# Optimization experiments

Measured on AMD Instinct MI355X. Metric: run time of the kernel, lower is better.

Reference implementation:

```python
import jax, jax.numpy as jnp
import numpy as np

N = 50000
E = 800000
F_IN = 1433
H = 256
C = 7


def setup_inputs() -> dict:
    key = jax.random.key(0)
    ks = jax.random.split(key, 8)
    x = jax.random.normal(ks[0], (N, F_IN), dtype=jnp.float32)
    edge_index = jax.random.randint(ks[1], (2, E), 0, N, dtype=jnp.int32)
    # glorot init for linear weights
    def glorot(k, fan_in, fan_out):
        s = jnp.sqrt(6.0 / (fan_in + fan_out)).astype(jnp.float32)
        return jax.random.uniform(k, (fan_in, fan_out), jnp.float32, -s, s)
    W1 = glorot(ks[2], F_IN, H)
    W2 = glorot(ks[3], H, H)
    W3 = glorot(ks[4], H, C)
    b1 = jnp.zeros((H,), jnp.float32)
    b2 = jnp.zeros((H,), jnp.float32)
    b3 = jnp.zeros((C,), jnp.float32)
    return {"x": x, "edge_index": edge_index, "W1": W1, "b1": b1,
            "W2": W2, "b2": b2, "W3": W3, "b3": b3}


def _gcn_norm(edge_index, num_nodes):
    # add self-loops, edge_weight = 1, symmetric normalization
    row = jnp.concatenate([edge_index[0], jnp.arange(num_nodes, dtype=edge_index.dtype)])
    col = jnp.concatenate([edge_index[1], jnp.arange(num_nodes, dtype=edge_index.dtype)])
    w = jnp.ones(row.shape[0], dtype=jnp.float32)
    deg = jax.ops.segment_sum(w, col, num_segments=num_nodes)  # degree on target (col)
    dinv = jnp.where(deg > 0, jax.lax.rsqrt(deg), 0.0)
    norm = dinv[row] * dinv[col]  # [E+N]
    return row, col, norm


def _gcn_layer(x, W, b, row, col, norm, num_nodes):
    h = x @ W                                   # [N, F_out]
    msg = h[row] * norm[:, None]                # gather + scale, [E+N, F_out]
    out = jax.ops.segment_sum(msg, col, num_segments=num_nodes)  # scatter-add
    return out + b


def reference(x, edge_index, W1, b1, W2, b2, W3, b3):
    row, col, norm = _gcn_norm(edge_index, N)
    h = jax.nn.relu(_gcn_layer(x, W1, b1, row, col, norm, N))
    h = jax.nn.relu(_gcn_layer(h, W2, b2, row, col, norm, N))
    h = _gcn_layer(h, W3, b3, row, col, norm, N)
    return jax.nn.log_softmax(h, axis=1)
```

## Files before the change

kernel.cpp:

```cpp
#include <hip/hip_runtime.h>
#include <math.h>

#define NNODES 50000
#define NEDGES 800000
#define FIN    1433
#define KP1    1472
#define HDIM   256
#define NCLS   7
#define MPAD   50048

typedef __attribute__((ext_vector_type(8))) short short8;
typedef __attribute__((ext_vector_type(4))) float f32x4;

__device__ __forceinline__ unsigned short f2bf(float f) {
    unsigned u = __builtin_bit_cast(unsigned, f);
    u += 0x7fffu + ((u >> 16) & 1u);
    return (unsigned short)(u >> 16);
}

__device__ __forceinline__ float bf2f(unsigned short u) {
    unsigned v = ((unsigned)u) << 16;
    return __builtin_bit_cast(float, v);
}

__device__ __forceinline__ void gl2lds16(const void* g, void* l) {
    __builtin_amdgcn_global_load_lds(
        (const __attribute__((address_space(1))) unsigned int*)g,
        (__attribute__((address_space(3))) unsigned int*)l, 16, 0, 0);
}

__device__ __forceinline__ f32x4 ld4u(const float* p) {
    f32x4 v; __builtin_memcpy(&v, p, 16); return v;
}


__global__ void count_kernel(const int* __restrict__ col, int* __restrict__ cnt, int E) {
    int e = blockIdx.x * blockDim.x + threadIdx.x;
    if (e < E) atomicAdd(&cnt[col[e]], 1);
}

#define SCAN_BS 512

__global__ __launch_bounds__(SCAN_BS) void scan_part(const int* __restrict__ cnt,
                                                     int* __restrict__ bsum, int n) {
    __shared__ int red[SCAN_BS];
    int t = threadIdx.x;
    int i = blockIdx.x * SCAN_BS + t;
    red[t] = (i < n) ? cnt[i] : 0;
    __syncthreads();
    for (int off = SCAN_BS / 2; off > 0; off >>= 1) {
        if (t < off) red[t] += red[t + off];
        __syncthreads();
    }
    if (t == 0) bsum[blockIdx.x] = red[0];
}

__global__ __launch_bounds__(128) void scan_top(int* __restrict__ bsum, int nb) {
    __shared__ int s[128];
    int t = threadIdx.x;
    int v = (t < nb) ? bsum[t] : 0;
    s[t] = v;
    __syncthreads();
    for (int off = 1; off < 128; off <<= 1) {
        int u = (t >= off) ? s[t - off] : 0;
        __syncthreads();
        s[t] += u;
        __syncthreads();
    }
    if (t < nb) bsum[t] = s[t] - v;
}

__global__ __launch_bounds__(SCAN_BS) void scan_apply(const int* __restrict__ cnt,
                                                      const int* __restrict__ bsum,
                                                      int* __restrict__ rp,
                                                      float* __restrict__ dinv,
                                                      int n, int total) {
    __shared__ int s[SCAN_BS];
    int t = threadIdx.x;
    int i = blockIdx.x * SCAN_BS + t;
    int v = (i < n) ? cnt[i] : 0;
    s[t] = v;
    __syncthreads();
    for (int off = 1; off < SCAN_BS; off <<= 1) {
        int u = (t >= off) ? s[t - off] : 0;
        __syncthreads();
        s[t] += u;
        __syncthreads();
    }
    if (i < n) {
        rp[i] = bsum[blockIdx.x] + s[t] - v;
        dinv[i] = rsqrtf((float)(v + 1));
    }
    if (i == n) rp[n] = total;
}

__global__ void fill_kernel(const int* __restrict__ row, const int* __restrict__ col,
                            const int* __restrict__ rp, int* __restrict__ cur,
                            int2* __restrict__ csrw,
                            const float* __restrict__ dinv, int E) {
    int e = blockIdx.x * blockDim.x + threadIdx.x;
    if (e < E) {
        int c = col[e], r = row[e];
        int pos = rp[c] + atomicAdd(&cur[c], 1);
        csrw[pos] = make_int2(r, __float_as_int(dinv[r] * dinv[c]));
    }
}


__global__ void cast_wt2(const float* __restrict__ W1, const float* __restrict__ W2,
                         unsigned short* __restrict__ w1t, unsigned short* __restrict__ w2t) {
    int idx = blockIdx.x * blockDim.x + threadIdx.x;
    if (idx < HDIM * KP1) {
        int n = idx / KP1, k = idx % KP1;
        w1t[idx] = f2bf((k < FIN) ? W1[(size_t)k * HDIM + n] : 0.f);
    } else {
        int j = idx - HDIM * KP1;
        if (j < HDIM * HDIM) {
            int n = j / HDIM, k = j % HDIM;
            w2t[j] = f2bf(W2[(size_t)k * HDIM + n]);
        }
    }
}


__global__ __launch_bounds__(256) void gemm1_fused(const float* __restrict__ X,
                                                   const unsigned short* __restrict__ Bt,
                                                   unsigned short* __restrict__ C) {
    __shared__ __align__(16) unsigned short As[64 * 64];
    __shared__ __align__(16) unsigned short Bs[256 * 64];
    const int tid = threadIdx.x;
    const int wave = tid >> 6, lane = tid & 63;
    const int m0 = blockIdx.x * 64;
    const int wn = wave * 64;
    const int kq = lane >> 4, l16 = lane & 15;
    const int lq = lane >> 4;
    const int h  = lane & 15;

    int rowbase[4];
    #pragma unroll
    for (int i = 0; i < 4; ++i) {
        int r = m0 + wave * 16 + i * 4 + lq;
        if (r >= NNODES) r = NNODES - 1;
        rowbase[i] = r * FIN;
    }
    int aw[4];
    #pragma unroll
    for (int i = 0; i < 4; ++i) {
        int r7 = lq + 4 * (i & 1);
        aw[i] = (wave * 16 + i * 4 + lq) * 64 + (((h >> 1) ^ r7) * 8) + (h & 1) * 4;
    }

    int bo[8];
    #pragma unroll
    for (int i = 0; i < 8; ++i) {
        int c = i * 256 + tid;
        int n = c >> 3, ccg = (c & 7) ^ (n & 7);
        bo[i] = n * KP1 + ccg * 8;
    }

    int aoffb[2], boffb[2];
    #pragma unroll
    for (int ks = 0; ks < 2; ++ks) {
        int swz = ((ks * 4 + kq) ^ (l16 & 7)) * 8;
        aoffb[ks] = l16 * 64 + swz;
        boffb[ks] = (wn + l16) * 64 + swz;
    }

    f32x4 acc[4][4] = {};
    constexpr int NT = KP1 / 64;

    f32x4 fv[4];
    #pragma unroll
    for (int i = 0; i < 4; ++i) fv[i] = ld4u(&X[rowbase[i] + h * 4]);

    for (int t = 0; t < NT; ++t) {
        const int k0 = t * 64;
        #pragma unroll
        for (int i = 0; i < 8; ++i)
            gl2lds16(Bt + bo[i] + k0, &Bs[(i * 256 + tid) * 8]);
        #pragma unroll
        for (int i = 0; i < 4; ++i) {
            ushort4 pk = make_ushort4(f2bf(fv[i].x), f2bf(fv[i].y),
                                      f2bf(fv[i].z), f2bf(fv[i].w));
            *(ushort4*)&As[aw[i]] = pk;
        }
        __syncthreads();

        f32x4 nv[4];
        const bool more = (t + 1 < NT);
        if (more) {
            const int kb = k0 + 64 + h * 4;
            if (t + 2 == NT) {
                #pragma unroll
                for (int i = 0; i < 4; ++i) {
                    float a = (kb + 0 < FIN) ? X[rowbase[i] + kb + 0] : 0.f;
                    float b = (kb + 1 < FIN) ? X[rowbase[i] + kb + 1] : 0.f;
                    float c = (kb + 2 < FIN) ? X[rowbase[i] + kb + 2] : 0.f;
                    float d = (kb + 3 < FIN) ? X[rowbase[i] + kb + 3] : 0.f;
                    nv[i] = (f32x4){a, b, c, d};
                }
            } else {
                #pragma unroll
                for (int i = 0; i < 4; ++i) nv[i] = ld4u(&X[rowbase[i] + kb]);
            }
        }

        #pragma unroll
        for (int ks = 0; ks < 2; ++ks) {
            short8 af[4], bg[4];
            #pragma unroll
            for (int i = 0; i < 4; ++i) af[i] = *(const short8*)&As[i * 1024 + aoffb[ks]];
            #pragma unroll
            for (int j = 0; j < 4; ++j) bg[j] = *(const short8*)&Bs[j * 1024 + boffb[ks]];
            #pragma unroll
            for (int i = 0; i < 4; ++i)
                #pragma unroll
                for (int j = 0; j < 4; ++j)
                    acc[i][j] = __builtin_amdgcn_mfma_f32_16x16x32_bf16(af[i], bg[j], acc[i][j], 0, 0, 0);
        }
        __syncthreads();
        if (more) {
            #pragma unroll
            for (int i = 0; i < 4; ++i) fv[i] = nv[i];
        }
    }

    #pragma unroll
    for (int i = 0; i < 4; ++i) {
        int gm_base = m0 + i * 16 + (lane >> 4) * 4;
        #pragma unroll
        for (int r = 0; r < 4; ++r) {
            int gm = gm_base + r;
            if (gm < NNODES) {
                #pragma unroll
                for (int j = 0; j < 4; ++j) {
                    int gn = wn + j * 16 + l16;
                    C[(size_t)gm * HDIM + gn] = f2bf(acc[i][j][r]);
                }
            }
        }
    }
}


__global__ __launch_bounds__(256) void gemm2_lds(const unsigned short* __restrict__ A,
                                                 const unsigned short* __restrict__ Bt,
                                                 unsigned short* __restrict__ C) {
    __shared__ __align__(16) unsigned short As[64 * 64];
    __shared__ __align__(16) unsigned short Bs[256 * 64];
    const int tid = threadIdx.x;
    const int wave = tid >> 6, lane = tid & 63;
    const int m0 = blockIdx.x * 64;
    const int wn = wave * 64;
    const int kq = lane >> 4, l16 = lane & 15;

    int ao[2];
    #pragma unroll
    for (int i = 0; i < 2; ++i) {
        int c = i * 256 + tid;
        int m = c >> 3, ccg = (c & 7) ^ (m & 7);
        ao[i] = (m0 + m) * HDIM + ccg * 8;
    }
    int bo[8];
    #pragma unroll
    for (int i = 0; i < 8; ++i) {
        int c = i * 256 + tid;
        int n = c >> 3, ccg = (c & 7) ^ (n & 7);
        bo[i] = n * HDIM + ccg * 8;
    }
    int aoffb[2], boffb[2];
    #pragma unroll
    for (int ks = 0; ks < 2; ++ks) {
        int swz = ((ks * 4 + kq) ^ (l16 & 7)) * 8;
        aoffb[ks] = l16 * 64 + swz;
        boffb[ks] = (wn + l16) * 64 + swz;
    }

    f32x4 acc[4][4] = {};
    #pragma unroll
    for (int k0 = 0; k0 < HDIM; k0 += 64) {
        #pragma unroll
        for (int i = 0; i < 2; ++i) gl2lds16(A + ao[i] + k0, &As[(i * 256 + tid) * 8]);
        #pragma unroll
        for (int i = 0; i < 8; ++i) gl2lds16(Bt + bo[i] + k0, &Bs[(i * 256 + tid) * 8]);
        __syncthreads();
        #pragma unroll
        for (int ks = 0; ks < 2; ++ks) {
            short8 af[4], bg[4];
            #pragma unroll
            for (int i = 0; i < 4; ++i) af[i] = *(const short8*)&As[i * 1024 + aoffb[ks]];
            #pragma unroll
            for (int j = 0; j < 4; ++j) bg[j] = *(const short8*)&Bs[j * 1024 + boffb[ks]];
            #pragma unroll
            for (int i = 0; i < 4; ++i)
                #pragma unroll
                for (int j = 0; j < 4; ++j)
                    acc[i][j] = __builtin_amdgcn_mfma_f32_16x16x32_bf16(af[i], bg[j], acc[i][j], 0, 0, 0);
        }
        __syncthreads();
    }

    #pragma unroll
    for (int i = 0; i < 4; ++i) {
        int gm_base = m0 + i * 16 + (lane >> 4) * 4;
        #pragma unroll
        for (int r = 0; r < 4; ++r) {
            int gm = gm_base + r;
            if (gm < NNODES) {
                #pragma unroll
                for (int j = 0; j < 4; ++j) {
                    int gn = wn + j * 16 + l16;
                    C[(size_t)gm * HDIM + gn] = f2bf(acc[i][j][r]);
                }
            }
        }
    }
}


__device__ __forceinline__ void aggregate_row(const ushort4* __restrict__ h, int lane,
                                              int p, int p1,
                                              const int2* __restrict__ csrw,
                                              float& ax, float& ay, float& az, float& aw) {
    for (; p + 8 <= p1; p += 8) {
        int2 e[8];
        #pragma unroll
        for (int j = 0; j < 8; ++j) e[j] = csrw[p + j];
        ushort4 t[8];
        #pragma unroll
        for (int j = 0; j < 8; ++j) t[j] = h[e[j].x * 64 + lane];
        #pragma unroll
        for (int j = 0; j < 8; ++j) {
            float w = __int_as_float(e[j].y);
            ax += w * bf2f(t[j].x); ay += w * bf2f(t[j].y);
            az += w * bf2f(t[j].z); aw += w * bf2f(t[j].w);
        }
    }
    if (p + 4 <= p1) {
        int2 e[4];
        #pragma unroll
        for (int j = 0; j < 4; ++j) e[j] = csrw[p + j];
        ushort4 t[4];
        #pragma unroll
        for (int j = 0; j < 4; ++j) t[j] = h[e[j].x * 64 + lane];
        #pragma unroll
        for (int j = 0; j < 4; ++j) {
            float w = __int_as_float(e[j].y);
            ax += w * bf2f(t[j].x); ay += w * bf2f(t[j].y);
            az += w * bf2f(t[j].z); aw += w * bf2f(t[j].w);
        }
        p += 4;
    }
    for (; p < p1; ++p) {
        int2 e = csrw[p];
        float w = __int_as_float(e.y);
        ushort4 t = h[e.x * 64 + lane];
        ax += w * bf2f(t.x); ay += w * bf2f(t.y); az += w * bf2f(t.z); aw += w * bf2f(t.w);
    }
}


__global__ __launch_bounds__(256) void agg_kernel(const ushort4* __restrict__ h,
                                                  ushort4* __restrict__ out,
                                                  const float* __restrict__ dinv,
                                                  const int* __restrict__ rp,
                                                  const int2* __restrict__ csrw,
                                                  const float* __restrict__ bias,
                                                  int n) {
    int node = blockIdx.x * 4 + (threadIdx.x >> 6);
    int lane = threadIdx.x & 63;
    if (node >= n) return;
    float di = dinv[node];
    float sw = di * di;
    ushort4 hv = h[node * 64 + lane];
    float ax = sw * bf2f(hv.x), ay = sw * bf2f(hv.y);
    float az = sw * bf2f(hv.z), aw = sw * bf2f(hv.w);
    aggregate_row(h, lane, rp[node], rp[node + 1], csrw, ax, ay, az, aw);
    float4 b = ((const float4*)bias)[lane];
    ax = fmaxf(ax + b.x, 0.f); ay = fmaxf(ay + b.y, 0.f);
    az = fmaxf(az + b.z, 0.f); aw = fmaxf(aw + b.w, 0.f);
    out[node * 64 + lane] = make_ushort4(f2bf(ax), f2bf(ay), f2bf(az), f2bf(aw));
}


__global__ __launch_bounds__(256) void agg2_mm3_kernel(const ushort4* __restrict__ h,
                                                       float* __restrict__ h3,
                                                       const float* __restrict__ dinv,
                                                       const int* __restrict__ rp,
                                                       const int2* __restrict__ csrw,
                                                       const float* __restrict__ bias,
                                                       const float* __restrict__ W3,
                                                       int n) {
    __shared__ __align__(16) float Ws[NCLS * HDIM];
    int tid = threadIdx.x;
    for (int i = tid; i < NCLS * HDIM; i += 256)
        Ws[i] = W3[(i & 255) * NCLS + (i >> 8)];
    __syncthreads();

    int node = blockIdx.x * 4 + (tid >> 6);
    int lane = tid & 63;
    if (node >= n) return;
    float di = dinv[node];
    float sw = di * di;
    ushort4 hv = h[node * 64 + lane];
    float ax = sw * bf2f(hv.x), ay = sw * bf2f(hv.y);
    float az = sw * bf2f(hv.z), aw = sw * bf2f(hv.w);
    aggregate_row(h, lane, rp[node], rp[node + 1], csrw, ax, ay, az, aw);
    float4 b = ((const float4*)bias)[lane];
    ax = fmaxf(ax + b.x, 0.f); ay = fmaxf(ay + b.y, 0.f);
    az = fmaxf(az + b.z, 0.f); aw = fmaxf(aw + b.w, 0.f);

    float p7[NCLS];
    #pragma unroll
    for (int c = 0; c < NCLS; ++c) {
        float4 w4 = *(const float4*)&Ws[c * HDIM + 4 * lane];
        p7[c] = ax * w4.x + ay * w4.y + az * w4.z + aw * w4.w;
    }
    #pragma unroll
    for (int c = 0; c < NCLS; ++c)
        for (int off = 32; off > 0; off >>= 1) p7[c] += __shfl_down(p7[c], off);
    if (lane == 0) {
        #pragma unroll
        for (int c = 0; c < NCLS; ++c) h3[node * NCLS + c] = p7[c];
    }
}


__global__ void final_kernel(const float* __restrict__ h3, const float* __restrict__ dinv,
                             const int* __restrict__ rp, const int2* __restrict__ csrw,
                             const float* __restrict__ b3, float* __restrict__ out, int n) {
    int i = blockIdx.x * blockDim.x + threadIdx.x;
    if (i >= n) return;
    float di = dinv[i];
    float sw = di * di;
    float acc[NCLS];
    #pragma unroll
    for (int c = 0; c < NCLS; ++c) acc[c] = sw * h3[i * NCLS + c];
    int p = rp[i], p1 = rp[i + 1];
    for (; p + 4 <= p1; p += 4) {
        int2 e0 = csrw[p], e1 = csrw[p + 1], e2 = csrw[p + 2], e3 = csrw[p + 3];
        float w0 = __int_as_float(e0.y), w1 = __int_as_float(e1.y);
        float w2 = __int_as_float(e2.y), w3 = __int_as_float(e3.y);
        #pragma unroll
        for (int c = 0; c < NCLS; ++c)
            acc[c] += w0 * h3[e0.x * NCLS + c] + w1 * h3[e1.x * NCLS + c]
                    + w2 * h3[e2.x * NCLS + c] + w3 * h3[e3.x * NCLS + c];
    }
    for (; p < p1; ++p) {
        int2 e = csrw[p];
        float wg = __int_as_float(e.y);
        #pragma unroll
        for (int c = 0; c < NCLS; ++c) acc[c] += wg * h3[e.x * NCLS + c];
    }
    float mx = -1e30f;
    #pragma unroll
    for (int c = 0; c < NCLS; ++c) { acc[c] += b3[c]; mx = fmaxf(mx, acc[c]); }
    float sum = 0.f;
    #pragma unroll
    for (int c = 0; c < NCLS; ++c) sum += expf(acc[c] - mx);
    float lse = mx + logf(sum);
    #pragma unroll
    for (int c = 0; c < NCLS; ++c) out[i * NCLS + c] = acc[c] - lse;
}


extern "C" void kernel_launch(void* const* d_in, const int* in_sizes, int n_in,
                              void* d_out, int out_size, void* d_ws, size_t ws_size,
                              hipStream_t stream) {
    const float* x  = (const float*)d_in[0];
    const int*   ei = (const int*)d_in[1];
    const float* W1 = (const float*)d_in[2];
    const float* b1 = (const float*)d_in[3];
    const float* W2 = (const float*)d_in[4];
    const float* b2 = (const float*)d_in[5];
    const float* W3 = (const float*)d_in[6];
    const float* b3 = (const float*)d_in[7];
    float* out = (float*)d_out;
    const int* row = ei;
    const int* col = ei + NEDGES;

    char* w = (char*)d_ws;
    auto alloc = [&](size_t b) { void* p = (void*)w; w += (b + 255) & ~(size_t)255; return p; };
    int*   cnt  = (int*)alloc(NNODES * 4);
    int*   cur  = (int*)alloc(NNODES * 4);
    int*   rp   = (int*)alloc((NNODES + 1) * 4);
    float* dinv = (float*)alloc(NNODES * 4);
    int*   bsum = (int*)alloc(128 * 4);
    int2*  csrw = (int2*)alloc((size_t)NEDGES * 8);
    unsigned short* w1t  = (unsigned short*)alloc((size_t)HDIM * KP1 * 2);
    unsigned short* w2t  = (unsigned short*)alloc((size_t)HDIM * HDIM * 2);
    unsigned short* h_bf = (unsigned short*)alloc((size_t)MPAD * HDIM * 2);
    unsigned short* a_bf = (unsigned short*)alloc((size_t)MPAD * HDIM * 2);
    float* h3 = (float*)alloc((size_t)NNODES * NCLS * 4);

    const size_t cpad = ((size_t)NNODES * 4 + 255) & ~(size_t)255;
    hipMemsetAsync(cnt, 0, cpad + (size_t)NNODES * 4, stream);

    count_kernel<<<(NEDGES + 255) / 256, 256, 0, stream>>>(col, cnt, NEDGES);
    const int nsb = (NNODES + SCAN_BS - 1) / SCAN_BS;
    scan_part <<<nsb, SCAN_BS, 0, stream>>>(cnt, bsum, NNODES);
    scan_top  <<<1, 128, 0, stream>>>(bsum, nsb);
    scan_apply<<<nsb, SCAN_BS, 0, stream>>>(cnt, bsum, rp, dinv, NNODES, NEDGES);
    fill_kernel<<<(NEDGES + 255) / 256, 256, 0, stream>>>(row, col, rp, cur, csrw, dinv, NEDGES);

    cast_wt2<<<(HDIM * KP1 + HDIM * HDIM + 255) / 256, 256, 0, stream>>>(W1, W2, w1t, w2t);

    gemm1_fused<<<MPAD / 64, 256, 0, stream>>>(x, w1t, h_bf);
    agg_kernel<<<(NNODES + 3) / 4, 256, 0, stream>>>((const ushort4*)h_bf, (ushort4*)a_bf,
                                                     dinv, rp, csrw, b1, NNODES);
    gemm2_lds<<<MPAD / 64, 256, 0, stream>>>(a_bf, w2t, h_bf);
    agg2_mm3_kernel<<<(NNODES + 3) / 4, 256, 0, stream>>>((const ushort4*)h_bf, h3,
                                                          dinv, rp, csrw, b2, W3, NNODES);
    final_kernel<<<(NNODES + 255) / 256, 256, 0, stream>>>(h3, dinv, rp, csrw, b3, out, NNODES);
}
```

Baseline: 676.8 us.

## Double-buffer GEMM1 LDS tiles, merge count and weight-cast kernels, widen aggregation unroll

The first GEMM now keeps two LDS buffers for its A and B tiles, issuing the next tile's async global-to-LDS loads and bf16 conversion while MFMAs run on the current tile. It also prefetches X two tiles ahead. The edge-count kernel and the weight transpose-cast kernel are merged into one launch to save a kernel launch. The aggregation loop is unrolled to 16 edges to put more gathers in flight. Costs are double the LDS per block (about 80KB), which may reduce occupancy, and higher register pressure in the aggregation kernels.

Measured after the change: 679.6 us. No clear change (+0.4%).

```diff
diff --git a/kernel.cpp b/kernel.cpp
--- a/kernel.cpp
+++ b/kernel.cpp
@@ -34,9 +34,29 @@
 }
 
 
-__global__ void count_kernel(const int* __restrict__ col, int* __restrict__ cnt, int E) {
-    int e = blockIdx.x * blockDim.x + threadIdx.x;
-    if (e < E) atomicAdd(&cnt[col[e]], 1);
+#define NB_COUNT 3125
+#define NB_CAST  1728
+
+__global__ void count_cast(const int* __restrict__ col, int* __restrict__ cnt,
+                           const float* __restrict__ W1, const float* __restrict__ W2,
+                           unsigned short* __restrict__ w1t, unsigned short* __restrict__ w2t) {
+    int b = blockIdx.x;
+    if (b < NB_COUNT) {
+        int e = b * 256 + threadIdx.x;
+        if (e < NEDGES) atomicAdd(&cnt[col[e]], 1);
+    } else {
+        int idx = (b - NB_COUNT) * 256 + threadIdx.x;
+        if (idx < HDIM * KP1) {
+            int n = idx / KP1, k = idx % KP1;
+            w1t[idx] = f2bf((k < FIN) ? W1[(size_t)k * HDIM + n] : 0.f);
+        } else {
+            int j = idx - HDIM * KP1;
+            if (j < HDIM * HDIM) {
+                int n = j / HDIM, k = j % HDIM;
+                w2t[j] = f2bf(W2[(size_t)k * HDIM + n]);
+            }
+        }
+    }
 }
 
 #define SCAN_BS 512
@@ -107,27 +127,11 @@
 }
 
 
-__global__ void cast_wt2(const float* __restrict__ W1, const float* __restrict__ W2,
-                         unsigned short* __restrict__ w1t, unsigned short* __restrict__ w2t) {
-    int idx = blockIdx.x * blockDim.x + threadIdx.x;
-    if (idx < HDIM * KP1) {
-        int n = idx / KP1, k = idx % KP1;
-        w1t[idx] = f2bf((k < FIN) ? W1[(size_t)k * HDIM + n] : 0.f);
-    } else {
-        int j = idx - HDIM * KP1;
-        if (j < HDIM * HDIM) {
-            int n = j / HDIM, k = j % HDIM;
-            w2t[j] = f2bf(W2[(size_t)k * HDIM + n]);
-        }
-    }
-}
-
-
 __global__ __launch_bounds__(256) void gemm1_fused(const float* __restrict__ X,
                                                    const unsigned short* __restrict__ Bt,
                                                    unsigned short* __restrict__ C) {
-    __shared__ __align__(16) unsigned short As[64 * 64];
-    __shared__ __align__(16) unsigned short Bs[256 * 64];
+    __shared__ __align__(16) unsigned short As[2][64 * 64];
+    __shared__ __align__(16) unsigned short Bs[2][256 * 64];
     const int tid = threadIdx.x;
     const int wave = tid >> 6, lane = tid & 63;
     const int m0 = blockIdx.x * 64;
@@ -169,49 +173,60 @@
     f32x4 acc[4][4] = {};
     constexpr int NT = KP1 / 64;
 
-    f32x4 fv[4];
-    #pragma unroll
-    for (int i = 0; i < 4; ++i) fv[i] = ld4u(&X[rowbase[i] + h * 4]);
-
+    f32x4 cur4[4], nxt[4];
+    #pragma unroll
+    for (int i = 0; i < 4; ++i) cur4[i] = ld4u(&X[rowbase[i] + h * 4]);
+    #pragma unroll
+    for (int i = 0; i < 8; ++i)
+        gl2lds16(Bt + bo[i], &Bs[0][(i * 256 + tid) * 8]);
+    #pragma unroll
+    for (int i = 0; i < 4; ++i) {
+        ushort4 pk = make_ushort4(f2bf(cur4[i].x), f2bf(cur4[i].y),
+                                  f2bf(cur4[i].z), f2bf(cur4[i].w));
+        *(ushort4*)&As[0][aw[i]] = pk;
+    }
+    #pragma unroll
+    for (int i = 0; i < 4; ++i) nxt[i] = ld4u(&X[rowbase[i] + 64 + h * 4]);
+    __syncthreads();
+
+    int c = 0;
     for (int t = 0; t < NT; ++t) {
-        const int k0 = t * 64;
-        #pragma unroll
-        for (int i = 0; i < 8; ++i)
-            gl2lds16(Bt + bo[i] + k0, &Bs[(i * 256 + tid) * 8]);
-        #pragma unroll
-        for (int i = 0; i < 4; ++i) {
-            ushort4 pk = make_ushort4(f2bf(fv[i].x), f2bf(fv[i].y),
-                                      f2bf(fv[i].z), f2bf(fv[i].w));
-            *(ushort4*)&As[aw[i]] = pk;
-        }
-        __syncthreads();
-
-        f32x4 nv[4];
-        const bool more = (t + 1 < NT);
-        if (more) {
-            const int kb = k0 + 64 + h * 4;
-            if (t + 2 == NT) {
+        f32x4 tmp[4];
+        const bool have2 = (t + 2 < NT);
+        if (have2) {
+            const int kb = (t + 2) * 64 + h * 4;
+            if (t + 2 == NT - 1) {
                 #pragma unroll
                 for (int i = 0; i < 4; ++i) {
                     float a = (kb + 0 < FIN) ? X[rowbase[i] + kb + 0] : 0.f;
                     float b = (kb + 1 < FIN) ? X[rowbase[i] + kb + 1] : 0.f;
-                    float c = (kb + 2 < FIN) ? X[rowbase[i] + kb + 2] : 0.f;
-                    float d = (kb + 3 < FIN) ? X[rowbase[i] + kb + 3] : 0.f;
-                    nv[i] = (f32x4){a, b, c, d};
+                    float d = (kb + 2 < FIN) ? X[rowbase[i] + kb + 2] : 0.f;
+                    float e = (kb + 3 < FIN) ? X[rowbase[i] + kb + 3] : 0.f;
+                    tmp[i] = (f32x4){a, b, d, e};
                 }
             } else {
                 #pragma unroll
-                for (int i = 0; i < 4; ++i) nv[i] = ld4u(&X[rowbase[i] + kb]);
+                for (int i = 0; i < 4; ++i) tmp[i] = ld4u(&X[rowbase[i] + kb]);
             }
         }
-
+        if (t + 1 < NT) {
+            #pragma unroll
+            for (int i = 0; i < 8; ++i)
+                gl2lds16(Bt + bo[i] + (t + 1) * 64, &Bs[c ^ 1][(i * 256 + tid) * 8]);
+            #pragma unroll
+            for (int i = 0; i < 4; ++i) {
+                ushort4 pk = make_ushort4(f2bf(nxt[i].x), f2bf(nxt[i].y),
+                                          f2bf(nxt[i].z), f2bf(nxt[i].w));
+                *(ushort4*)&As[c ^ 1][aw[i]] = pk;
+            }
+        }
         #pragma unroll
         for (int ks = 0; ks < 2; ++ks) {
             short8 af[4], bg[4];
             #pragma unroll
-            for (int i = 0; i < 4; ++i) af[i] = *(const short8*)&As[i * 1024 + aoffb[ks]];
-            #pragma unroll
-            for (int j = 0; j < 4; ++j) bg[j] = *(const short8*)&Bs[j * 1024 + boffb[ks]];
+            for (int i = 0; i < 4; ++i) af[i] = *(const short8*)&As[c][i * 1024 + aoffb[ks]];
+            #pragma unroll
+            for (int j = 0; j < 4; ++j) bg[j] = *(const short8*)&Bs[c][j * 1024 + boffb[ks]];
             #pragma unroll
             for (int i = 0; i < 4; ++i)
                 #pragma unroll
@@ -219,10 +234,11 @@
                     acc[i][j] = __builtin_amdgcn_mfma_f32_16x16x32_bf16(af[i], bg[j], acc[i][j], 0, 0, 0);
         }
         __syncthreads();
-        if (more) {
-            #pragma unroll
-            for (int i = 0; i < 4; ++i) fv[i] = nv[i];
-        }
+        if (have2) {
+            #pragma unroll
+            for (int i = 0; i < 4; ++i) nxt[i] = tmp[i];
+        }
+        c ^= 1;
     }
 
     #pragma unroll
@@ -322,21 +338,21 @@
                                               int p, int p1,
                                               const int2* __restrict__ csrw,
                                               float& ax, float& ay, float& az, float& aw) {
-    for (; p + 8 <= p1; p += 8) {
-        int2 e[8];
-        #pragma unroll
-        for (int j = 0; j < 8; ++j) e[j] = csrw[p + j];
-        ushort4 t[8];
-        #pragma unroll
-        for (int j = 0; j < 8; ++j) t[j] = h[e[j].x * 64 + lane];
-        #pragma unroll
-        for (int j = 0; j < 8; ++j) {
+    for (; p + 16 <= p1; p += 16) {
+        int2 e[16];
+        #pragma unroll
+        for (int j = 0; j < 16; ++j) e[j] = csrw[p + j];
+        ushort4 t[16];
+        #pragma unroll
+        for (int j = 0; j < 16; ++j) t[j] = h[e[j].x * 64 + lane];
+        #pragma unroll
+        for (int j = 0; j < 16; ++j) {
             float w = __int_as_float(e[j].y);
             ax += w * bf2f(t[j].x); ay += w * bf2f(t[j].y);
             az += w * bf2f(t[j].z); aw += w * bf2f(t[j].w);
         }
     }
-    if (p + 4 <= p1) {
+    for (; p + 4 <= p1; p += 4) {
         int2 e[4];
         #pragma unroll
         for (int j = 0; j < 4; ++j) e[j] = csrw[p + j];
@@ -349,7 +365,6 @@
             ax += w * bf2f(t[j].x); ay += w * bf2f(t[j].y);
             az += w * bf2f(t[j].z); aw += w * bf2f(t[j].w);
         }
-        p += 4;
     }
     for (; p < p1; ++p) {
         int2 e = csrw[p];
@@ -496,14 +511,12 @@
     const size_t cpad = ((size_t)NNODES * 4 + 255) & ~(size_t)255;
     hipMemsetAsync(cnt, 0, cpad + (size_t)NNODES * 4, stream);
 
-    count_kernel<<<(NEDGES + 255) / 256, 256, 0, stream>>>(col, cnt, NEDGES);
+    count_cast<<<NB_COUNT + NB_CAST, 256, 0, stream>>>(col, cnt, W1, W2, w1t, w2t);
     const int nsb = (NNODES + SCAN_BS - 1) / SCAN_BS;
     scan_part <<<nsb, SCAN_BS, 0, stream>>>(cnt, bsum, NNODES);
     scan_top  <<<1, 128, 0, stream>>>(bsum, nsb);
     scan_apply<<<nsb, SCAN_BS, 0, stream>>>(cnt, bsum, rp, dinv, NNODES, NEDGES);
     fill_kernel<<<(NEDGES + 255) / 256, 256, 0, stream>>>(row, col, rp, cur, csrw, dinv, NEDGES);
-
-    cast_wt2<<<(HDIM * KP1 + HDIM * HDIM + 255) / 256, 256, 0, stream>>>(W1, W2, w1t, w2t);
 
     gemm1_fused<<<MPAD / 64, 256, 0, stream>>>(x, w1t, h_bf);
     agg_kernel<<<(NNODES + 3) / 4, 256, 0, stream>>>((const ushort4*)h_bf, (ushort4*)a_bf,
```
